# Optimization experiments

Hardware: AMD Instinct MI355X
Metric: run time of the kernel (lower is better)

The kernel has to match this reference:

```python
import jax, jax.numpy as jnp
import numpy as np

B, T, C = 1, 2048, 1024
H = 16
HD = C // H
BLOCK = 2048
NEG = float('-inf')

def setup_inputs() -> dict:
    key = jax.random.key(0)
    ks = jax.random.split(key, 6)
    x = jax.random.normal(ks[0], (B, T, C), dtype=jnp.float32)
    cumulative_scores = jax.random.normal(ks[1], (B, T), dtype=jnp.float32) * 0.1
    padding_mask = jnp.ones((B, T), dtype=jnp.float32)
    token_index = jax.random.randint(ks[2], (B, T), 0, BLOCK).astype(jnp.int64)
    w_attn = jax.random.normal(ks[3], (C, 3 * C), dtype=jnp.float32) * (1.0 / np.sqrt(C))
    b_attn = jnp.zeros((3 * C,), dtype=jnp.float32)
    w_proj = jax.random.normal(ks[4], (C, C), dtype=jnp.float32) * (1.0 / np.sqrt(C))
    b_proj = jnp.zeros((C,), dtype=jnp.float32)
    return dict(x=x, cumulative_scores=cumulative_scores, padding_mask=padding_mask,
                token_index=token_index, w_attn=w_attn, b_attn=b_attn,
                w_proj=w_proj, b_proj=b_proj)

def _rotate_half(z):
    z1, z2 = z[..., : z.shape[-1] // 2], z[..., z.shape[-1] // 2 :]
    return jnp.concatenate((-z2, z1), axis=-1)

def reference(x, cumulative_scores, padding_mask, token_index, w_attn, b_attn, w_proj, b_proj):
    # fused QKV projection
    qkv = x @ w_attn + b_attn                      # (B,T,3C)
    q, k, v = jnp.split(qkv, 3, axis=2)
    q = q.reshape(B, T, H, HD).transpose(0, 2, 1, 3)  # (B,H,T,HD)
    k = k.reshape(B, T, H, HD).transpose(0, 2, 1, 3)
    v = v.reshape(B, T, H, HD).transpose(0, 2, 1, 3)

    # dynamic per-token RoPE positions: global token counts (original scatter
    # broadcasts indices over batch, so counts are global across all batches)
    cnt = jnp.zeros((BLOCK,), jnp.float32).at[token_index.reshape(-1)].add(1.0)
    per_tok = (1.0 / (cnt + 1e-10))[token_index]       # (B,T)
    partial = jnp.cumsum(per_tok, axis=-1)             # (B,T) fractional positions

    inv_freq = 1.0 / (10000.0 ** (jnp.arange(0, HD, 2, dtype=jnp.float32) / HD))
    freqs = partial[..., None] * inv_freq              # (B,T,HD/2)
    emb = jnp.concatenate((freqs, freqs), axis=-1)     # (B,T,HD)
    cos = jnp.cos(emb)[:, None]                        # (B,1,T,HD)
    sin = jnp.sin(emb)[:, None]
    q = q * cos + _rotate_half(q) * sin
    k = k * cos + _rotate_half(k) * sin

    # 'fork' plan: overwrite last channel
    q = q.at[..., -1].set(1.0)
    k = k.at[..., -1].set(jnp.broadcast_to(cumulative_scores[:, None, :], (B, H, T)))

    # additive causal + padding mask (B,T,T)
    causal = jnp.where(jnp.tril(jnp.ones((T, T), jnp.bool_)), 0.0, NEG)
    pm = jnp.take_along_axis(padding_mask, token_index, axis=1)     # (B,T)
    outer = pm[:, :, None] * pm[:, None, :]
    pad_add = jnp.where(outer.astype(jnp.bool_), 0.0, NEG)
    mask = causal[None, :, :] + pad_add                              # (B,T,T)

    # scale v by exp(cumulative_scores)
    v = v * jnp.exp(cumulative_scores)[:, None, :, None]

    scores = jnp.einsum('bhqd,bhkd->bhqk', q, k) / np.sqrt(HD) + mask[:, None]
    probs = jax.nn.softmax(scores, axis=-1)
    y = jnp.einsum('bhqk,bhkd->bhqd', probs, v)        # (B,H,T,HD)
    y = y.transpose(0, 2, 1, 3).reshape(B, T, C)
    return y @ w_proj + b_proj
```

## Files before the change

### kernel.cpp

```cpp
#include <hip/hip_runtime.h>
#include <math.h>

#define T 2048
#define C 1024
#define H 16
#define HD 64
#define N3 (3*C)
#define NBLOCK 2048

typedef __attribute__((ext_vector_type(8))) short bf16x8;
typedef __attribute__((ext_vector_type(4))) float f32x4;

#define MFMA16(a, b, c) __builtin_amdgcn_mfma_f32_16x16x32_bf16((a), (b), (c), 0, 0, 0)

__device__ inline short f2bf(float f) {
    unsigned u; __builtin_memcpy(&u, &f, 4);
    unsigned r = (u + 0x7fffu + ((u >> 16) & 1u)) >> 16;
    return (short)r;
}
__device__ inline float bf2f(short s) {
    unsigned u = ((unsigned)(unsigned short)s) << 16;
    float f; __builtin_memcpy(&f, &u, 4);
    return f;
}

__device__ inline void gload_lds16(const void* g, void* l) {
    __builtin_amdgcn_global_load_lds((const __attribute__((address_space(1))) unsigned int*)g,
                                     (__attribute__((address_space(3))) unsigned int*)l,
                                     16, 0, 0);
}

__global__ __launch_bounds__(256) void pre_kernel(const float* __restrict__ x,
                                                  const float* __restrict__ w_attn,
                                                  const float* __restrict__ w_proj,
                                                  const int* __restrict__ tok,
                                                  const float* __restrict__ padmask,
                                                  short* __restrict__ xb,
                                                  short* __restrict__ wabT,
                                                  short* __restrict__ wpbT,
                                                  float* __restrict__ partial,
                                                  float* __restrict__ pm_tok) {
    int bid = blockIdx.x;
    int tid = threadIdx.x;
    if (bid == 3072) {
        __shared__ float cntS[NBLOCK];
        __shared__ float sums[256];
        #pragma unroll
        for (int j = 0; j < 8; ++j) cntS[tid * 8 + j] = 0.0f;
        __syncthreads();
        int tk[8];
        #pragma unroll
        for (int j = 0; j < 8; ++j) {
            tk[j] = tok[tid * 8 + j];
            atomicAdd(&cntS[tk[j]], 1.0f);
        }
        __syncthreads();
        float vals[8];
        float s = 0.0f;
        #pragma unroll
        for (int j = 0; j < 8; ++j) {
            s += 1.0f / (cntS[tk[j]] + 1e-10f);
            vals[j] = s;
            pm_tok[tid * 8 + j] = padmask[tk[j]];
        }
        sums[tid] = s;
        __syncthreads();
        for (int off = 1; off < 256; off <<= 1) {
            float v = (tid >= off) ? sums[tid - off] : 0.0f;
            __syncthreads();
            sums[tid] += v;
            __syncthreads();
        }
        float offset = (tid > 0) ? sums[tid - 1] : 0.0f;
        #pragma unroll
        for (int j = 0; j < 8; ++j) partial[tid * 8 + j] = offset + vals[j];
        return;
    }
    if (bid < 2048) {
        int i = bid * 1024 + tid * 4;
        float4 v = *(const float4*)(x + i);
        short4 o;
        o.x = f2bf(v.x); o.y = f2bf(v.y); o.z = f2bf(v.z); o.w = f2bf(v.w);
        *(short4*)(xb + i) = o;
        return;
    }
    __shared__ float S[64][65];
    const float* in; short* out; int Kd, Nd, bx, by;
    if (bid < 2816) {
        int b = bid - 2048;
        bx = b % 48; by = b / 48;
        in = w_attn; out = wabT; Kd = C; Nd = N3;
    } else {
        int b = bid - 2816;
        bx = b % 16; by = b / 16;
        in = w_proj; out = wpbT; Kd = C; Nd = C;
    }
    int n0 = bx * 64, k0 = by * 64;
    #pragma unroll
    for (int i = 0; i < 16; ++i) {
        int lin = tid + i * 256;
        int r = lin >> 6, c = lin & 63;
        S[r][c] = in[(size_t)(k0 + r) * Nd + n0 + c];
    }
    __syncthreads();
    #pragma unroll
    for (int i = 0; i < 16; ++i) {
        int lin = tid + i * 256;
        int rn = lin >> 6, ck = lin & 63;
        out[(size_t)(n0 + rn) * Kd + k0 + ck] = f2bf(S[ck][rn]);
    }
}

template <int OUT_BF16, int EPI>
__global__ __launch_bounds__(256) void gemm_bt64(const short* __restrict__ A,
                                                 const short* __restrict__ Bt,
                                                 const float* __restrict__ bias,
                                                 void* __restrict__ Cout,
                                                 int M, int N, int K,
                                                 const float* __restrict__ partial,
                                                 const float* __restrict__ cumsc,
                                                 const float* __restrict__ pm_tok,
                                                 short* __restrict__ vbT) {
    __shared__ alignas(16) short As[2][64 * 32];
    __shared__ alignas(16) short Bs[2][128 * 32];
    int tid = threadIdx.x;
    int m0 = blockIdx.y * 64, n0 = blockIdx.x * 128;
    int w = tid >> 6, l = tid & 63;
    int wm = (w >> 1) * 32, wn = (w & 1) * 64;
    int lq = l & 15, g = l >> 4;
    int prow = l >> 2, pcol = (l & 3) * 8;
    f32x4 acc[2][4] = {};
    for (int k0 = 0; k0 < K; k0 += 64) {
        #pragma unroll
        for (int hf = 0; hf < 2; ++hf) {
            int kk = k0 + hf * 32;
            int rowA = w * 16 + prow;
            gload_lds16(A + (size_t)(m0 + rowA) * K + kk + pcol, As[hf] + w * 512);
            #pragma unroll
            for (int i = 0; i < 2; ++i) {
                int c = w * 2 + i;
                int row = c * 16 + prow;
                gload_lds16(Bt + (size_t)(n0 + row) * K + kk + pcol, Bs[hf] + c * 512);
            }
        }
        __syncthreads();
        #pragma unroll
        for (int hf = 0; hf < 2; ++hf) {
            bf16x8 af[2], bfr[4];
            #pragma unroll
            for (int f = 0; f < 2; ++f)
                af[f] = *(const bf16x8*)(As[hf] + (wm + f * 16 + lq) * 32 + g * 8);
            #pragma unroll
            for (int j = 0; j < 4; ++j)
                bfr[j] = *(const bf16x8*)(Bs[hf] + (wn + j * 16 + lq) * 32 + g * 8);
            #pragma unroll
            for (int fi = 0; fi < 2; ++fi)
                #pragma unroll
                for (int fj = 0; fj < 4; ++fj)
                    acc[fi][fj] = MFMA16(af[fi], bfr[fj], acc[fi][fj]);
        }
        __syncthreads();
    }

    if (EPI == 0) {
        #pragma unroll
        for (int fi = 0; fi < 2; ++fi)
            #pragma unroll
            for (int fj = 0; fj < 4; ++fj)
                #pragma unroll
                for (int r = 0; r < 4; ++r) {
                    int m = m0 + wm + fi * 16 + g * 4 + r;
                    int n = n0 + wn + fj * 16 + lq;
                    float v = acc[fi][fj][r] + bias[n];
                    if (OUT_BF16) ((short*)Cout)[(size_t)m * N + n] = f2bf(v);
                    else          ((float*)Cout)[(size_t)m * N + n] = v;
                }
    } else {
        short* Cb = (short*)Cout;
        int cb = n0 + wn;
        int section = cb >> 10;
        float b0 = bias[cb + lq],      b1 = bias[cb + 16 + lq];
        float b2 = bias[cb + 32 + lq], b3 = bias[cb + 48 + lq];
        if (section < 2) {
            bool isQ = (section == 0);
            float inv0 = exp2f(-(float)lq * (13.287712379549449f / 32.0f));
            float inv1 = exp2f(-(float)(lq + 16) * (13.287712379549449f / 32.0f));
            #pragma unroll
            for (int fi = 0; fi < 2; ++fi)
                #pragma unroll
                for (int r = 0; r < 4; ++r) {
                    int trow = m0 + wm + fi * 16 + g * 4 + r;
                    float pt = partial[trow];
                    float sn0, cs0, sn1, cs1;
                    __sincosf(pt * inv0, &sn0, &cs0);
                    __sincosf(pt * inv1, &sn1, &cs1);
                    float a0 = acc[fi][0][r] + b0;
                    float a1 = acc[fi][1][r] + b1;
                    float a2 = acc[fi][2][r] + b2;
                    float a3 = acc[fi][3][r] + b3;
                    float lo0 = a0 * cs0 - a2 * sn0;
                    float hi0 = a2 * cs0 + a0 * sn0;
                    float lo1 = a1 * cs1 - a3 * sn1;
                    float hi1 = a3 * cs1 + a1 * sn1;
                    if (lq == 15) {
                        float pm = pm_tok[trow];
                        hi1 = isQ ? ((pm != 0.0f) ? 1.0f : 0.0f)
                                  : ((pm != 0.0f) ? cumsc[trow] : -1e20f);
                    }
                    size_t base = (size_t)trow * N3 + cb;
                    Cb[base + lq]      = f2bf(lo0);
                    Cb[base + 16 + lq] = f2bf(lo1);
                    Cb[base + 32 + lq] = f2bf(hi0);
                    Cb[base + 48 + lq] = f2bf(hi1);
                }
        } else {
            int h = (cb - 2 * C) >> 6;
            #pragma unroll
            for (int fi = 0; fi < 2; ++fi) {
                int tb = m0 + wm + fi * 16 + g * 4;
                float ef[4];
                #pragma unroll
                for (int r = 0; r < 4; ++r) ef[r] = __expf(cumsc[tb + r]);
                #pragma unroll
                for (int fj = 0; fj < 4; ++fj) {
                    int d = fj * 16 + lq;
                    float bv = (fj == 0) ? b0 : (fj == 1) ? b1 : (fj == 2) ? b2 : b3;
                    short4 o;
                    o.x = f2bf((acc[fi][fj][0] + bv) * ef[0]);
                    o.y = f2bf((acc[fi][fj][1] + bv) * ef[1]);
                    o.z = f2bf((acc[fi][fj][2] + bv) * ef[2]);
                    o.w = f2bf((acc[fi][fj][3] + bv) * ef[3]);
                    *(short4*)(vbT + (size_t)(h * 64 + d) * T + tb) = o;
                }
            }
        }
    }
}

__global__ __launch_bounds__(256) void attn_flash(const short* __restrict__ qkvb,
                                                  const short* __restrict__ vbT,
                                                  short* __restrict__ yb) {
    __shared__ alignas(16) short Kt[2][64 * 64];
    __shared__ alignas(16) short Vt[2][64 * 64];
    __shared__ alignas(16) short Ps[4][16][72];

    int b = blockIdx.x;
    int h, qt;
    if (b < 256) { h = b & 15; qt = 31 - (b >> 4); }
    else         { int c2 = b - 256; h = c2 & 15; qt = c2 >> 4; }
    int tid = threadIdx.x;
    int w = tid >> 6, l = tid & 63;
    int lq = l & 15, g = l >> 4;
    int qrl = w * 16 + lq;

    const short* qbase = qkvb + (size_t)(qt * 64 + qrl) * N3 + h * 64;
    bf16x8 qf0 = *(const bf16x8*)(qbase + g * 8);
    bf16x8 qf1 = *(const bf16x8*)(qbase + 32 + g * 8);

    f32x4 accO[4] = {};
    float lsum = 0.0f;

    int srow = tid >> 3, scol = (tid & 7) * 8;
    const short* kgb = qkvb + C + h * 64 + scol;
    const short* vgb = vbT + (size_t)(h * 64) * T + scol;
    int wb0 = srow * 128 + ((scol * 2) ^ ((srow & 7) << 4));
    int wb1 = (srow + 32) * 128 + ((scol * 2) ^ ((srow & 7) << 4));

    auto do_tile = [&](int cur, bool masked) {
        const char* Kc = (const char*)Kt[cur];
        const char* Vc = (const char*)Vt[cur];
        f32x4 s[4] = {};
        __builtin_amdgcn_s_setprio(1);
        #pragma unroll
        for (int f = 0; f < 4; ++f) {
            int row = f * 16 + lq;
            const char* kr_ = Kc + row * 128;
            int sw = (row & 7) << 4;
            bf16x8 a0 = *(const bf16x8*)(kr_ + ((g * 16) ^ sw));
            bf16x8 a1 = *(const bf16x8*)(kr_ + ((64 + g * 16) ^ sw));
            s[f] = MFMA16(a0, qf0, s[f]);
            s[f] = MFMA16(a1, qf1, s[f]);
        }
        __builtin_amdgcn_s_setprio(0);
        float p[16];
        #pragma unroll
        for (int f = 0; f < 4; ++f)
            #pragma unroll
            for (int r = 0; r < 4; ++r) {
                float sv = s[f][r] * 0.125f;
                if (masked) {
                    int kl = f * 16 + g * 4 + r;
                    sv = (kl > qrl) ? -INFINITY : sv;
                }
                float pv = __expf(sv);
                p[f * 4 + r] = pv;
                lsum += pv;
            }
        #pragma unroll
        for (int f = 0; f < 4; ++f) {
            unsigned u0, u1;
            asm("v_cvt_pk_bf16_f32 %0, %1, %2" : "=v"(u0) : "v"(p[f * 4 + 0]), "v"(p[f * 4 + 1]));
            asm("v_cvt_pk_bf16_f32 %0, %1, %2" : "=v"(u1) : "v"(p[f * 4 + 2]), "v"(p[f * 4 + 3]));
            uint2 uu; uu.x = u0; uu.y = u1;
            *(uint2*)&Ps[w][lq][f * 16 + g * 4] = uu;
        }
        __builtin_amdgcn_s_setprio(1);
        #pragma unroll
        for (int kh = 0; kh < 2; ++kh) {
            bf16x8 pa = *(const bf16x8*)&Ps[w][lq][kh * 32 + g * 8];
            #pragma unroll
            for (int f = 0; f < 4; ++f) {
                int vrow = f * 16 + lq;
                const char* vr_ = Vc + vrow * 128;
                bf16x8 vb = *(const bf16x8*)(vr_ + (((kh * 32 + g * 8) * 2) ^ ((vrow & 7) << 4)));
                accO[f] = MFMA16(pa, vb, accO[f]);
            }
        }
        __builtin_amdgcn_s_setprio(0);
    };

    uint4 kr0 = *(const uint4*)(kgb + (size_t)srow * N3);
    uint4 kr1 = *(const uint4*)(kgb + (size_t)(srow + 32) * N3);
    uint4 vr0 = *(const uint4*)(vgb + (size_t)srow * T);
    uint4 vr1 = *(const uint4*)(vgb + (size_t)(srow + 32) * T);
    *(uint4*)((char*)Kt[0] + wb0) = kr0;
    *(uint4*)((char*)Kt[0] + wb1) = kr1;
    *(uint4*)((char*)Vt[0] + wb0) = vr0;
    *(uint4*)((char*)Vt[0] + wb1) = vr1;
    __syncthreads();

    for (int t = 0; t < qt; ++t) {
        int kn = (t + 1) * 64;
        kr0 = *(const uint4*)(kgb + (size_t)(kn + srow) * N3);
        kr1 = *(const uint4*)(kgb + (size_t)(kn + srow + 32) * N3);
        vr0 = *(const uint4*)(vgb + (size_t)srow * T + kn);
        vr1 = *(const uint4*)(vgb + (size_t)(srow + 32) * T + kn);

        do_tile(t & 1, false);

        int nxt = (t & 1) ^ 1;
        *(uint4*)((char*)Kt[nxt] + wb0) = kr0;
        *(uint4*)((char*)Kt[nxt] + wb1) = kr1;
        *(uint4*)((char*)Vt[nxt] + wb0) = vr0;
        *(uint4*)((char*)Vt[nxt] + wb1) = vr1;
        __syncthreads();
    }
    do_tile(qt & 1, true);

    lsum += __shfl_xor(lsum, 16);
    lsum += __shfl_xor(lsum, 32);
    float linv_own = 1.0f / lsum;
    float li[4];
    #pragma unroll
    for (int r = 0; r < 4; ++r) li[r] = __shfl(linv_own, g * 4 + r);

    #pragma unroll
    for (int f = 0; f < 4; ++f)
        #pragma unroll
        for (int r = 0; r < 4; ++r) {
            int trow = qt * 64 + w * 16 + g * 4 + r;
            yb[(size_t)trow * C + h * 64 + f * 16 + lq] = f2bf(accO[f][r] * li[r]);
        }
}

extern "C" void kernel_launch(void* const* d_in, const int* in_sizes, int n_in,
                              void* d_out, int out_size, void* d_ws, size_t ws_size,
                              hipStream_t stream) {
    const float* x       = (const float*)d_in[0];
    const float* cumsc   = (const float*)d_in[1];
    const float* padmask = (const float*)d_in[2];
    const int*   tok     = (const int*)d_in[3];
    const float* w_attn  = (const float*)d_in[4];
    const float* b_attn  = (const float*)d_in[5];
    const float* w_proj  = (const float*)d_in[6];
    const float* b_proj  = (const float*)d_in[7];
    float* out = (float*)d_out;

    float* part   = (float*)d_ws;
    float* pm_tok = part + 2048;
    short* xb     = (short*)(pm_tok + 2048);
    short* wabT   = xb + (size_t)T * C;
    short* wpbT   = wabT + (size_t)N3 * C;
    short* qkvb   = wpbT + (size_t)C * C;
    short* vbT    = qkvb + (size_t)T * N3;
    short* yb     = vbT + (size_t)C * T;

    pre_kernel<<<3073, 256, 0, stream>>>(x, w_attn, w_proj, tok, padmask,
                                         xb, wabT, wpbT, part, pm_tok);
    gemm_bt64<1, 1><<<dim3(N3 / 128, T / 64), 256, 0, stream>>>(
        xb, wabT, b_attn, qkvb, T, N3, C, part, cumsc, pm_tok, vbT);
    attn_flash<<<512, 256, 0, stream>>>(qkvb, vbT, yb);
    gemm_bt64<0, 0><<<dim3(C / 128, T / 64), 256, 0, stream>>>(
        yb, wpbT, b_proj, out, T, C, C, nullptr, nullptr, nullptr, nullptr);
}
```

Baseline: 85.70 us.

## Split attention KV range across two wave groups per block and merge partials

Each attention block now runs 512 threads as two groups of four waves, and each group processes half of the causal KV tiles for the same 64-row query tile using its own double-buffered LDS. The second group's partial outputs and row sums are then added into the first group's through shared memory before normalization. The goal is to halve the serial KV loop length and balance the long causal tiles. The cost is doubled LDS, an extra merge step, and lower occupancy per block. The merge adds sums directly with no max rescaling, which is valid only because the softmax already omits the running max.

```diff
diff --git a/kernel.cpp b/kernel.cpp
--- a/kernel.cpp
+++ b/kernel.cpp
@@ -237,12 +237,12 @@
     }
 }
 
-__global__ __launch_bounds__(256) void attn_flash(const short* __restrict__ qkvb,
+__global__ __launch_bounds__(512) void attn_flash(const short* __restrict__ qkvb,
                                                   const short* __restrict__ vbT,
                                                   short* __restrict__ yb) {
-    __shared__ alignas(16) short Kt[2][64 * 64];
-    __shared__ alignas(16) short Vt[2][64 * 64];
-    __shared__ alignas(16) short Ps[4][16][72];
+    __shared__ alignas(16) short Kt[2][2][64 * 64];
+    __shared__ alignas(16) short Vt[2][2][64 * 64];
+    __shared__ alignas(16) short Ps[8][16][72];
 
     int b = blockIdx.x;
     int h, qt;
@@ -250,8 +250,13 @@
     else         { int c2 = b - 256; h = c2 & 15; qt = c2 >> 4; }
     int tid = threadIdx.x;
     int w = tid >> 6, l = tid & 63;
+    int gi = w >> 2, wl = w & 3;
     int lq = l & 15, g = l >> 4;
-    int qrl = w * 16 + lq;
+    int qrl = wl * 16 + lq;
+
+    int mid = (qt + 2) >> 1;
+    int tbase = gi ? mid : 0;
+    int cnt = gi ? (qt - mid + 1) : mid;
 
     const short* qbase = qkvb + (size_t)(qt * 64 + qrl) * N3 + h * 64;
     bf16x8 qf0 = *(const bf16x8*)(qbase + g * 8);
@@ -260,15 +265,31 @@
     f32x4 accO[4] = {};
     float lsum = 0.0f;
 
-    int srow = tid >> 3, scol = (tid & 7) * 8;
+    int t256 = tid & 255;
+    int srow = t256 >> 3, scol = (t256 & 7) * 8;
     const short* kgb = qkvb + C + h * 64 + scol;
     const short* vgb = vbT + (size_t)(h * 64) * T + scol;
     int wb0 = srow * 128 + ((scol * 2) ^ ((srow & 7) << 4));
     int wb1 = (srow + 32) * 128 + ((scol * 2) ^ ((srow & 7) << 4));
 
-    auto do_tile = [&](int cur, bool masked) {
-        const char* Kc = (const char*)Kt[cur];
-        const char* Vc = (const char*)Vt[cur];
+    uint4 kr0, kr1, vr0, vr1;
+    auto stageRegs = [&](int tile) {
+        int kb = tile * 64;
+        kr0 = *(const uint4*)(kgb + (size_t)(kb + srow) * N3);
+        kr1 = *(const uint4*)(kgb + (size_t)(kb + srow + 32) * N3);
+        vr0 = *(const uint4*)(vgb + (size_t)srow * T + kb);
+        vr1 = *(const uint4*)(vgb + (size_t)(srow + 32) * T + kb);
+    };
+    auto writeLds = [&](int buf) {
+        *(uint4*)((char*)Kt[gi][buf] + wb0) = kr0;
+        *(uint4*)((char*)Kt[gi][buf] + wb1) = kr1;
+        *(uint4*)((char*)Vt[gi][buf] + wb0) = vr0;
+        *(uint4*)((char*)Vt[gi][buf] + wb1) = vr1;
+    };
+
+    auto do_tile = [&](int buf, bool masked) {
+        const char* Kc = (const char*)Kt[gi][buf];
+        const char* Vc = (const char*)Vt[gi][buf];
         f32x4 s[4] = {};
         __builtin_amdgcn_s_setprio(1);
         #pragma unroll
@@ -319,48 +340,53 @@
         __builtin_amdgcn_s_setprio(0);
     };
 
-    uint4 kr0 = *(const uint4*)(kgb + (size_t)srow * N3);
-    uint4 kr1 = *(const uint4*)(kgb + (size_t)(srow + 32) * N3);
-    uint4 vr0 = *(const uint4*)(vgb + (size_t)srow * T);
-    uint4 vr1 = *(const uint4*)(vgb + (size_t)(srow + 32) * T);
-    *(uint4*)((char*)Kt[0] + wb0) = kr0;
-    *(uint4*)((char*)Kt[0] + wb1) = kr1;
-    *(uint4*)((char*)Vt[0] + wb0) = vr0;
-    *(uint4*)((char*)Vt[0] + wb1) = vr1;
+    if (cnt > 0) { stageRegs(tbase); writeLds(0); }
     __syncthreads();
 
-    for (int t = 0; t < qt; ++t) {
-        int kn = (t + 1) * 64;
-        kr0 = *(const uint4*)(kgb + (size_t)(kn + srow) * N3);
-        kr1 = *(const uint4*)(kgb + (size_t)(kn + srow + 32) * N3);
-        vr0 = *(const uint4*)(vgb + (size_t)srow * T + kn);
-        vr1 = *(const uint4*)(vgb + (size_t)(srow + 32) * T + kn);
-
-        do_tile(t & 1, false);
-
-        int nxt = (t & 1) ^ 1;
-        *(uint4*)((char*)Kt[nxt] + wb0) = kr0;
-        *(uint4*)((char*)Kt[nxt] + wb1) = kr1;
-        *(uint4*)((char*)Vt[nxt] + wb0) = vr0;
-        *(uint4*)((char*)Vt[nxt] + wb1) = vr1;
-        __syncthreads();
-    }
-    do_tile(qt & 1, true);
+    for (int j = 0; j < mid; ++j) {
+        bool active = (j < cnt);
+        bool pf = (j + 1 < cnt);
+        if (pf) stageRegs(tbase + j + 1);
+        if (active) do_tile(j & 1, (tbase + j) == qt);
+        if (pf) writeLds((j & 1) ^ 1);
+        __syncthreads();
+    }
 
     lsum += __shfl_xor(lsum, 16);
     lsum += __shfl_xor(lsum, 32);
-    float linv_own = 1.0f / lsum;
-    float li[4];
-    #pragma unroll
-    for (int r = 0; r < 4; ++r) li[r] = __shfl(linv_own, g * 4 + r);
-
-    #pragma unroll
-    for (int f = 0; f < 4; ++f)
-        #pragma unroll
-        for (int r = 0; r < 4; ++r) {
-            int trow = qt * 64 + w * 16 + g * 4 + r;
-            yb[(size_t)trow * C + h * 64 + f * 16 + lq] = f2bf(accO[f][r] * li[r]);
-        }
+
+    float* depO = (float*)Kt[1];
+    float* depL = (float*)Vt[1];
+    if (gi == 1) {
+        #pragma unroll
+        for (int f = 0; f < 4; ++f)
+            #pragma unroll
+            for (int r = 0; r < 4; ++r)
+                depO[wl * 1024 + (g * 4 + r) * 64 + f * 16 + lq] = accO[f][r];
+        if (g == 0) depL[wl * 16 + lq] = lsum;
+    }
+    __syncthreads();
+    if (gi == 0) {
+        #pragma unroll
+        for (int f = 0; f < 4; ++f)
+            #pragma unroll
+            for (int r = 0; r < 4; ++r)
+                accO[f][r] += depO[wl * 1024 + (g * 4 + r) * 64 + f * 16 + lq];
+        lsum += depL[wl * 16 + lq];
+
+        float linv_own = 1.0f / lsum;
+        float li[4];
+        #pragma unroll
+        for (int r = 0; r < 4; ++r) li[r] = __shfl(linv_own, g * 4 + r);
+
+        #pragma unroll
+        for (int f = 0; f < 4; ++f)
+            #pragma unroll
+            for (int r = 0; r < 4; ++r) {
+                int trow = qt * 64 + wl * 16 + g * 4 + r;
+                yb[(size_t)trow * C + h * 64 + f * 16 + lq] = f2bf(accO[f][r] * li[r]);
+            }
+    }
 }
 
 extern "C" void kernel_launch(void* const* d_in, const int* in_sizes, int n_in,
@@ -389,7 +415,7 @@
                                          xb, wabT, wpbT, part, pm_tok);
     gemm_bt64<1, 1><<<dim3(N3 / 128, T / 64), 256, 0, stream>>>(
         xb, wabT, b_attn, qkvb, T, N3, C, part, cumsc, pm_tok, vbT);
-    attn_flash<<<512, 256, 0, stream>>>(qkvb, vbT, yb);
+    attn_flash<<<512, 512, 0, stream>>>(qkvb, vbT, yb);
     gemm_bt64<0, 0><<<dim3(C / 128, T / 64), 256, 0, stream>>>(
         yb, wpbT, b_proj, out, T, C, C, nullptr, nullptr, nullptr, nullptr);
 }
```

After: 88.99 us. +3.8%, slower.
